# Kernel tuning notes

Hardware: AMD Instinct MI355X
Metric: run time of the kernel (lower is better)

## Reference

```python
import jax, jax.numpy as jnp
import numpy as np

PATCH = 3
SIGMA2 = 0.5 ** 2
EPS = 1e-8


def _gauss_kernel():
    # depthwise Gaussian patch kernel, shape (6, 1, P, P, P), normalized to sum 1
    c = (PATCH - 1) / 2.0
    zz, yy, xx = np.meshgrid(np.arange(PATCH), np.arange(PATCH), np.arange(PATCH), indexing='ij')
    d2 = (xx - c) ** 2 + (yy - c) ** 2 + (zz - c) ** 2
    g = np.exp(-d2 / SIGMA2).astype(np.float32)
    g /= g.sum()
    k = np.zeros((6, 1, PATCH, PATCH, PATCH), np.float32)
    k[:, 0] = g
    return jnp.asarray(k)


def _shift(x, axis, step):
    # zero-padded shift: step=+1 -> out[i] = x[i+1]; step=-1 -> out[i] = x[i-1]
    n = x.shape[axis]
    pad = [(0, 0)] * x.ndim
    lo = 1 if step > 0 else 0
    pad[axis] = (0, 1) if step > 0 else (1, 0)
    xp = jnp.pad(x, pad)
    idx = [slice(None)] * x.ndim
    idx[axis] = slice(lo, lo + n)
    return xp[tuple(idx)]


def _mind(img):
    # shift-conv (one-hot 3x3x3 kernels) == 6 axis shifts: +z,-z,+y,-y,+x,-x
    shifted = jnp.concatenate([
        _shift(img, 2, 1), _shift(img, 2, -1),
        _shift(img, 3, 1), _shift(img, 3, -1),
        _shift(img, 4, 1), _shift(img, 4, -1),
    ], axis=1)                                  # (B,6,D,H,W)
    diff2 = (shifted - img) ** 2                # broadcast over channel dim
    gk = _gauss_kernel()
    Dp = jax.lax.conv_general_dilated(
        diff2, gk, window_strides=(1, 1, 1), padding='SAME',
        feature_group_count=6,
        dimension_numbers=('NCDHW', 'OIDHW', 'NCDHW'))  # depthwise Gaussian smoothing
    Vx = Dp.mean(axis=1, keepdims=True)
    num = jnp.exp(-Dp / (Vx + EPS))
    return num / (num.sum(axis=1, keepdims=True) + EPS)


def setup_inputs() -> dict:
    key = jax.random.key(0)
    img = jax.random.normal(key, (2, 1, 192, 192, 192), dtype=jnp.float32)
    return {"img": img}


def reference(img):
    return _mind(img)
```

## Files before the change

kernel.cpp:

```cpp
#include <hip/hip_runtime.h>

#define DHW   192
#define DHW2  (DHW*DHW)
#define TX    64
#define TTY   4
#define YB    4
#define BY    (TTY*YB)
#define ZCH   8
#define NT    (TX*TTY)
#define RY    (BY+4)
#define RXW   (TX+8)
#define SLICE (RY*RXW)
#define NF4   (SLICE/4)
#define ROWF4 (RXW/4)

__global__ __launch_bounds__(NT, 4)
void mind3d_kernel(const float* __restrict__ img, float* __restrict__ out)
{
    __shared__ float ring[4][SLICE];

    const int lane = threadIdx.x;
    const int ty   = threadIdx.y;
    const int tid  = ty*TX + lane;

    const int x0 = blockIdx.x * TX;
    const int y0 = blockIdx.y * BY;
    const int zi = blockIdx.z;
    const int nzc = DHW / ZCH;
    const int b  = zi / nzc;
    const int z0 = (zi - b*nzc) * ZCH;

    const float* imgb = img + (size_t)b * ((size_t)DHW * DHW2);

    const float a1 = 0.01831563889245986f;
    const float n1 = 1.0f/(1.0f + 2.0f*a1);
    const float norm3 = n1*n1*n1;

    const int gx = x0 + lane;
    const float mL = (gx == 0)     ? 0.f : 1.f;
    const float mR = (gx == DHW-1) ? 0.f : 1.f;
    const int wy = y0 + ty*YB;
    const int u  = lane + 4;

    const int r0  = tid / ROWF4, c0i = tid - r0*ROWF4;
    const int gy0s = y0 - 2 + r0, gx0s = x0 - 4 + (c0i << 2);
    const bool in0 = ((unsigned)gy0s < (unsigned)DHW) && ((unsigned)gx0s <= (unsigned)(DHW-4));
    const int t2  = tid + NT;
    const bool g2 = (t2 < NF4);
    const int r1  = t2 / ROWF4, c1i = t2 - r1*ROWF4;
    const int gy1s = y0 - 2 + r1, gx1s = x0 - 4 + (c1i << 2);
    const bool in1 = g2 && ((unsigned)gy1s < (unsigned)DHW) && ((unsigned)gx1s <= (unsigned)(DHW-4));

    float4 sv0, sv1;
    auto issue = [&](int z) {
        sv0 = float4{0.f,0.f,0.f,0.f};
        sv1 = float4{0.f,0.f,0.f,0.f};
        if ((unsigned)z < (unsigned)DHW) {
            const float* sp = imgb + (size_t)z * DHW2;
            if (in0) sv0 = *(const float4*)(sp + (size_t)gy0s*DHW + gx0s);
            if (in1) sv1 = *(const float4*)(sp + (size_t)gy1s*DHW + gx1s);
        }
    };
    auto commit = [&](int z) {
        float4* dst = (float4*)ring[(z + 8) & 3];
        dst[tid] = sv0;
        if (g2) dst[t2] = sv1;
    };

    float zm[YB][6], zc[YB][6], zS0[YB];
    #pragma unroll
    for (int j = 0; j < YB; ++j) {
        zS0[j] = 0.f;
        #pragma unroll
        for (int c = 0; c < 6; ++c) { zm[j][c] = 0.f; zc[j][c] = 0.f; }
    }

    issue(z0-2); commit(z0-2);
    issue(z0-1); commit(z0-1);
    issue(z0);   commit(z0);
    issue(z0+1);
    __syncthreads();

    for (int zs = z0 - 1; zs <= z0 + ZCH; ++zs) {
        if (zs + 2 <= z0 + ZCH + 1) commit(zs + 2);
        if (zs + 3 <= z0 + ZCH + 1) issue(zs + 3);

        const bool zok  = ((unsigned)zs < (unsigned)DHW);
        const bool warm = (zs == z0 - 1);
        const float* rcs = ring[(zs + 8) & 3] + ty*YB*RXW + u;
        const float* rps = ring[(zs + 9) & 3] + (ty*YB + 1)*RXW + u;
        const float* rms = ring[(zs + 7) & 3] + (ty*YB + 1)*RXW + u;

        float A1 = rcs[-1], A2 = rcs[0], A3 = rcs[1];
        float B0 = rcs[RXW-2], B1 = rcs[RXW-1], B2 = rcs[RXW], B3 = rcs[RXW+1], B4 = rcs[RXW+2];

        float T[3][6];
        const int zcout = zs - 1;
        const bool emitz = (zcout >= z0);

        #pragma unroll
        for (int k = 0; k < 6; ++k) {
            const int gr = wy - 1 + k;
            const float* rk = rcs + (k + 2)*RXW;
            float C0 = rk[-2], C1 = rk[-1], C2 = rk[0], C3 = rk[1], C4 = rk[2];
            const float* pk = rps + k*RXW;
            float zpL = pk[-1], zpC = pk[0], zpR = pk[1];

            const bool rowok = ((unsigned)gr < (unsigned)DHW);
            const bool rok   = zok && rowok;
            float* Tk = T[k % 3];

            {
                float eL = zpL-B1, eC = zpC-B2, eR = zpR-B3;
                Tk[0] = rowok ? (a1*(eL*eL*mL + eR*eR*mR) + eC*eC) : 0.f;
            }
            if (rok) {
                float d0 = B1-B0, d1 = B2-B1, d2 = B3-B2, d3 = B4-B3;
                float q0 = d0*d0, q1 = d1*d1, q2 = d2*d2, q3 = d3*d3;
                float eL, eC, eR;
                eL = C1-B1;  eC = C2-B2;  eR = C3-B3;
                Tk[2] = a1*(eL*eL*mL + eR*eR*mR) + eC*eC;
                eL = A1-B1;  eC = A2-B2;  eR = A3-B3;
                Tk[3] = a1*(eL*eL*mL + eR*eR*mR) + eC*eC;
                Tk[4] = a1*(q1*mL + q3*mR) + q2;
                Tk[5] = a1*(q0*mL + q2*mR) + q1;
            } else {
                Tk[2]=0.f; Tk[3]=0.f; Tk[4]=0.f; Tk[5]=0.f;
            }
            if (warm) {
                float t1v = 0.f;
                if (rok) {
                    const float* mk = rms + k*RXW;
                    float zmL = mk[-1], zmC = mk[0], zmR = mk[1];
                    float eL = zmL-B1, eC = zmC-B2, eR = zmR-B3;
                    t1v = a1*(eL*eL*mL + eR*eR*mR) + eC*eC;
                }
                Tk[1] = t1v;
            }

            if (k >= 2) {
                const int j = k - 2;
                float s0 = a1*(T[(k-2)%3][0] + T[k%3][0]) + T[(k-1)%3][0];
                float s2 = a1*(T[(k-2)%3][2] + T[k%3][2]) + T[(k-1)%3][2];
                float s3 = a1*(T[(k-2)%3][3] + T[k%3][3]) + T[(k-1)%3][3];
                float s4 = a1*(T[(k-2)%3][4] + T[k%3][4]) + T[(k-1)%3][4];
                float s5 = a1*(T[(k-2)%3][5] + T[k%3][5]) + T[(k-1)%3][5];
                float s1 = warm ? (a1*(T[(k-2)%3][1] + T[k%3][1]) + T[(k-1)%3][1])
                                : (zok ? zS0[j] : 0.f);
                zS0[j] = s0;
                float s0st = zok ? s0 : 0.f;
                float sp_[6] = {s0st, s1, s2, s3, s4, s5};

                if (emitz) {
                    float dp[6], sum = 0.f;
                    #pragma unroll
                    for (int c = 0; c < 6; ++c) {
                        dp[c] = norm3 * (a1*(zm[j][c] + sp_[c]) + zc[j][c]);
                        sum += dp[c];
                    }
                    float inv = 1.0f / (sum * (1.0f/6.0f) + 1e-8f);
                    float num[6], nsum = 0.f;
                    #pragma unroll
                    for (int c = 0; c < 6; ++c) {
                        num[c] = __expf(-dp[c] * inv);
                        nsum += num[c];
                    }
                    float rs = 1.0f / (nsum + 1e-8f);
                    size_t base = ((size_t)(6*b)*DHW + zcout) * (size_t)DHW2
                                + (size_t)(wy + j)*DHW + (size_t)gx;
                    #pragma unroll
                    for (int c = 0; c < 6; ++c)
                        out[base + (size_t)c * ((size_t)DHW*DHW2)] = num[c]*rs;
                }
                #pragma unroll
                for (int c = 0; c < 6; ++c) { zm[j][c] = zc[j][c]; zc[j][c] = sp_[c]; }
            }
            A1=B1; A2=B2; A3=B3;
            B0=C0; B1=C1; B2=C2; B3=C3; B4=C4;
        }
        __syncthreads();
    }
}

extern "C" void kernel_launch(void* const* d_in, const int* in_sizes, int n_in,
                              void* d_out, int out_size, void* d_ws, size_t ws_size,
                              hipStream_t stream)
{
    const float* img = (const float*)d_in[0];
    float* out = (float*)d_out;
    dim3 block(TX, TTY, 1);
    dim3 grid(DHW/TX, DHW/BY, 2*(DHW/ZCH));
    hipLaunchKernelGGL(mind3d_kernel, grid, block, 0, stream, img, out);
}
```

Baseline: 410.2 us.

## Replace shared-memory ring buffer with direct cached global loads and nontemporal stores

Removes the LDS ring buffer, the software-pipelined prefetch and the per-slice __syncthreads. Each thread now reads its stencil neighbours straight from global memory through clamped offsets and edge masks, and relies on L1/L2 for reuse across threads. Output stores become nontemporal so the write stream does not evict cached input. The trade is many more global load instructions per point in exchange for dropping barriers and LDS traffic.

```diff
diff --git a/kernel.cpp b/kernel.cpp
--- a/kernel.cpp
+++ b/kernel.cpp
@@ -8,20 +8,12 @@
 #define BY    (TTY*YB)
 #define ZCH   8
 #define NT    (TX*TTY)
-#define RY    (BY+4)
-#define RXW   (TX+8)
-#define SLICE (RY*RXW)
-#define NF4   (SLICE/4)
-#define ROWF4 (RXW/4)
 
 __global__ __launch_bounds__(NT, 4)
 void mind3d_kernel(const float* __restrict__ img, float* __restrict__ out)
 {
-    __shared__ float ring[4][SLICE];
-
     const int lane = threadIdx.x;
     const int ty   = threadIdx.y;
-    const int tid  = ty*TX + lane;
 
     const int x0 = blockIdx.x * TX;
     const int y0 = blockIdx.y * BY;
@@ -39,33 +31,19 @@
     const int gx = x0 + lane;
     const float mL = (gx == 0)     ? 0.f : 1.f;
     const float mR = (gx == DHW-1) ? 0.f : 1.f;
+    const float v2L = (gx >= 2)     ? 1.f : 0.f;
+    const float v1L = (gx >= 1)     ? 1.f : 0.f;
+    const float v1R = (gx <= DHW-2) ? 1.f : 0.f;
+    const float v2R = (gx <= DHW-3) ? 1.f : 0.f;
     const int wy = y0 + ty*YB;
-    const int u  = lane + 4;
 
-    const int r0  = tid / ROWF4, c0i = tid - r0*ROWF4;
-    const int gy0s = y0 - 2 + r0, gx0s = x0 - 4 + (c0i << 2);
-    const bool in0 = ((unsigned)gy0s < (unsigned)DHW) && ((unsigned)gx0s <= (unsigned)(DHW-4));
-    const int t2  = tid + NT;
-    const bool g2 = (t2 < NF4);
-    const int r1  = t2 / ROWF4, c1i = t2 - r1*ROWF4;
-    const int gy1s = y0 - 2 + r1, gx1s = x0 - 4 + (c1i << 2);
-    const bool in1 = g2 && ((unsigned)gy1s < (unsigned)DHW) && ((unsigned)gx1s <= (unsigned)(DHW-4));
-
-    float4 sv0, sv1;
-    auto issue = [&](int z) {
-        sv0 = float4{0.f,0.f,0.f,0.f};
-        sv1 = float4{0.f,0.f,0.f,0.f};
-        if ((unsigned)z < (unsigned)DHW) {
-            const float* sp = imgb + (size_t)z * DHW2;
-            if (in0) sv0 = *(const float4*)(sp + (size_t)gy0s*DHW + gx0s);
-            if (in1) sv1 = *(const float4*)(sp + (size_t)gy1s*DHW + gx1s);
-        }
-    };
-    auto commit = [&](int z) {
-        float4* dst = (float4*)ring[(z + 8) & 3];
-        dst[tid] = sv0;
-        if (g2) dst[t2] = sv1;
-    };
+    int vo[5];
+    #pragma unroll
+    for (int d = 0; d < 5; ++d) {
+        int xx = gx + d - 2;
+        xx = xx < 0 ? 0 : (xx > DHW-1 ? DHW-1 : xx);
+        vo[d] = wy*DHW + xx;
+    }
 
     float zm[YB][6], zc[YB][6], zS0[YB];
     #pragma unroll
@@ -75,24 +53,22 @@
         for (int c = 0; c < 6; ++c) { zm[j][c] = 0.f; zc[j][c] = 0.f; }
     }
 
-    issue(z0-2); commit(z0-2);
-    issue(z0-1); commit(z0-1);
-    issue(z0);   commit(z0);
-    issue(z0+1);
-    __syncthreads();
+    for (int zs = z0 - 1; zs <= z0 + ZCH; ++zs) {
+        const bool zok  = ((unsigned)zs < (unsigned)DHW);
+        const bool pok  = (zs + 1 < DHW);
+        const bool warm = (zs == z0 - 1);
+        const float* cs = imgb + (size_t)(zok ? zs : 0) * DHW2;
+        const float* ps = imgb + (size_t)(pok ? zs + 1 : 0) * DHW2;
+        const float* ms = imgb + (size_t)(z0 >= 2 ? z0 - 2 : 0) * DHW2;
 
-    for (int zs = z0 - 1; zs <= z0 + ZCH; ++zs) {
-        if (zs + 2 <= z0 + ZCH + 1) commit(zs + 2);
-        if (zs + 3 <= z0 + ZCH + 1) issue(zs + 3);
-
-        const bool zok  = ((unsigned)zs < (unsigned)DHW);
-        const bool warm = (zs == z0 - 1);
-        const float* rcs = ring[(zs + 8) & 3] + ty*YB*RXW + u;
-        const float* rps = ring[(zs + 9) & 3] + (ty*YB + 1)*RXW + u;
-        const float* rms = ring[(zs + 7) & 3] + (ty*YB + 1)*RXW + u;
-
-        float A1 = rcs[-1], A2 = rcs[0], A3 = rcs[1];
-        float B0 = rcs[RXW-2], B1 = rcs[RXW-1], B2 = rcs[RXW], B3 = rcs[RXW+1], B4 = rcs[RXW+2];
+        float A1, A2, A3, B0, B1, B2, B3, B4;
+        if (zok && wy - 2 >= 0) {
+            A1 = cs[vo[1] - 2*DHW]*v1L; A2 = cs[vo[2] - 2*DHW]; A3 = cs[vo[3] - 2*DHW]*v1R;
+        } else { A1 = 0.f; A2 = 0.f; A3 = 0.f; }
+        if (zok && wy - 1 >= 0) {
+            B0 = cs[vo[0] - DHW]*v2L; B1 = cs[vo[1] - DHW]*v1L; B2 = cs[vo[2] - DHW];
+            B3 = cs[vo[3] - DHW]*v1R; B4 = cs[vo[4] - DHW]*v2R;
+        } else { B0 = 0.f; B1 = 0.f; B2 = 0.f; B3 = 0.f; B4 = 0.f; }
 
         float T[3][6];
         const int zcout = zs - 1;
@@ -101,13 +77,21 @@
         #pragma unroll
         for (int k = 0; k < 6; ++k) {
             const int gr = wy - 1 + k;
-            const float* rk = rcs + (k + 2)*RXW;
-            float C0 = rk[-2], C1 = rk[-1], C2 = rk[0], C3 = rk[1], C4 = rk[2];
-            const float* pk = rps + k*RXW;
-            float zpL = pk[-1], zpC = pk[0], zpR = pk[1];
+            float C0, C1, C2, C3, C4;
+            if (zok && (wy + k) < DHW) {
+                C0 = cs[vo[0] + k*DHW]*v2L; C1 = cs[vo[1] + k*DHW]*v1L;
+                C2 = cs[vo[2] + k*DHW];
+                C3 = cs[vo[3] + k*DHW]*v1R; C4 = cs[vo[4] + k*DHW]*v2R;
+            } else { C0 = 0.f; C1 = 0.f; C2 = 0.f; C3 = 0.f; C4 = 0.f; }
+            float zpL, zpC, zpR;
+            const bool rowok = ((unsigned)gr < (unsigned)DHW);
+            if (pok && rowok) {
+                zpL = ps[vo[1] + (k-1)*DHW]*v1L;
+                zpC = ps[vo[2] + (k-1)*DHW];
+                zpR = ps[vo[3] + (k-1)*DHW]*v1R;
+            } else { zpL = 0.f; zpC = 0.f; zpR = 0.f; }
 
-            const bool rowok = ((unsigned)gr < (unsigned)DHW);
-            const bool rok   = zok && rowok;
+            const bool rok = zok && rowok;
             float* Tk = T[k % 3];
 
             {
@@ -130,9 +114,13 @@
             if (warm) {
                 float t1v = 0.f;
                 if (rok) {
-                    const float* mk = rms + k*RXW;
-                    float zmL = mk[-1], zmC = mk[0], zmR = mk[1];
-                    float eL = zmL-B1, eC = zmC-B2, eR = zmR-B3;
+                    float zmLv = 0.f, zmCv = 0.f, zmRv = 0.f;
+                    if (z0 >= 2) {
+                        zmLv = ms[vo[1] + (k-1)*DHW]*v1L;
+                        zmCv = ms[vo[2] + (k-1)*DHW];
+                        zmRv = ms[vo[3] + (k-1)*DHW]*v1R;
+                    }
+                    float eL = zmLv-B1, eC = zmCv-B2, eR = zmRv-B3;
                     t1v = a1*(eL*eL*mL + eR*eR*mR) + eC*eC;
                 }
                 Tk[1] = t1v;
@@ -170,7 +158,8 @@
                                 + (size_t)(wy + j)*DHW + (size_t)gx;
                     #pragma unroll
                     for (int c = 0; c < 6; ++c)
-                        out[base + (size_t)c * ((size_t)DHW*DHW2)] = num[c]*rs;
+                        __builtin_nontemporal_store(num[c]*rs,
+                            &out[base + (size_t)c * ((size_t)DHW*DHW2)]);
                 }
                 #pragma unroll
                 for (int c = 0; c < 6; ++c) { zm[j][c] = zc[j][c]; zc[j][c] = sp_[c]; }
@@ -178,7 +167,6 @@
             A1=B1; A2=B2; A3=B3;
             B0=C0; B1=C1; B2=C2; B3=C3; B4=C4;
         }
-        __syncthreads();
     }
 }
 
```

Result: slower. 536.8 us (+30.9%).
